# Kernel tuning notes

Hardware: AMD Instinct MI355X
Metric: run time of the kernel (lower is better)

The kernel has to match this reference:

```python
import jax, jax.numpy as jnp
import numpy as np

EPS = 1e-5  # torch BatchNorm1d default eps

def _bn_train(h, gamma, beta):
    # BatchNorm1d in training mode on [B, C] (L=1 after global pool):
    # stats over the batch axis, biased variance.
    mu = h.mean(axis=0)
    var = ((h - mu) ** 2).mean(axis=0)
    return (h - mu) * jax.lax.rsqrt(var + EPS) * gamma + beta

def setup_inputs() -> dict:
    key = jax.random.key(0)
    k_x, k_w1, k_w2 = jax.random.split(key, 3)
    B, C, L = 16, 256, 16384
    Cr = C // 2  # reduction = 2
    x = jax.random.normal(k_x, (B, C, L), dtype=jnp.float32)
    # Conv1d kernel_size=1, bias=False -> channel matmuls; kaiming-ish scale
    w1 = jax.random.normal(k_w1, (Cr, C), dtype=jnp.float32) * (1.0 / np.sqrt(C))
    w2 = jax.random.normal(k_w2, (C, Cr), dtype=jnp.float32) * (1.0 / np.sqrt(Cr))
    g1 = jnp.ones((Cr,), jnp.float32)
    b1 = jnp.zeros((Cr,), jnp.float32)
    g2 = jnp.ones((C,), jnp.float32)
    b2 = jnp.zeros((C,), jnp.float32)
    return {"x": x, "w1": w1, "g1": g1, "b1": b1, "w2": w2, "g2": g2, "b2": b2}

def reference(x, w1, g1, b1, w2, g2, b2):
    # x: [B, C, L]
    s = x.mean(axis=-1)                      # AdaptiveAvgPool1d(1) -> [B, C]
    h = jnp.einsum('bc,rc->br', s, w1)       # 1x1 conv squeeze -> [B, Cr]
    h = _bn_train(h, g1, b1)
    h = jax.nn.gelu(h, approximate=False)    # torch nn.GELU default (erf)
    h = jnp.einsum('br,cr->bc', h, w2)       # 1x1 conv excite -> [B, C]
    h = _bn_train(h, g2, b2)
    gate = jax.nn.sigmoid(h)                 # [B, C]
    return x * gate[:, :, None]              # broadcast multiply over L
```

## Files before the change

kernel.cpp:

```cpp
#include <hip/hip_runtime.h>
#include <math.h>

#define B 16
#define C 256
#define CR 128
#define L 16384
#define NROW (B * C)
#define THREADS 256
#define ITERS (L / 4 / THREADS)

__global__ __launch_bounds__(THREADS) void row_mean_kernel(
    const float* __restrict__ x, float* __restrict__ s) {
    const int row = blockIdx.x;
    const int t = threadIdx.x;
    const float4* xr = (const float4*)(x + (size_t)row * L);

    float acc = 0.0f;
#pragma unroll
    for (int i = 0; i < ITERS; ++i) {
        float4 v = xr[t + i * THREADS];
        acc += (v.x + v.y) + (v.z + v.w);
    }
#pragma unroll
    for (int off = 32; off > 0; off >>= 1) acc += __shfl_down(acc, off, 64);

    __shared__ float wsum[THREADS / 64];
    if ((t & 63) == 0) wsum[t >> 6] = acc;
    __syncthreads();
    if (t == 0) {
        float tot = 0.0f;
#pragma unroll
        for (int w = 0; w < THREADS / 64; ++w) tot += wsum[w];
        s[row] = tot * (1.0f / (float)L);
    }
}

__global__ __launch_bounds__(256) void mlp1_kernel(
    const float* __restrict__ s, const float* __restrict__ w1,
    const float* __restrict__ g1, const float* __restrict__ b1,
    float* __restrict__ h1) {
    const int r = blockIdx.x;
    const int t = threadIdx.x;
    const int b = t >> 4;
    const int j = t & 15;

    const float4* sv = (const float4*)(s + b * C) + j * 4;
    const float4* wv = (const float4*)(w1 + r * C) + j * 4;
    float acc = 0.0f;
#pragma unroll
    for (int k = 0; k < 4; ++k) {
        float4 a = sv[k], w = wv[k];
        acc += a.x * w.x + a.y * w.y + a.z * w.z + a.w * w.w;
    }
#pragma unroll
    for (int off = 8; off > 0; off >>= 1) acc += __shfl_down(acc, off, 16);

    __shared__ float h[B];
    if (j == 0) h[b] = acc;
    __syncthreads();

    float mu = 0.0f;
#pragma unroll
    for (int i = 0; i < B; ++i) mu += h[i];
    mu *= (1.0f / (float)B);
    float var = 0.0f;
#pragma unroll
    for (int i = 0; i < B; ++i) { float d = h[i] - mu; var = fmaf(d, d, var); }
    var *= (1.0f / (float)B);
    const float inv = rsqrtf(var + 1e-5f);

    if (t < B) {
        float v = (h[t] - mu) * inv * g1[r] + b1[r];
        v = 0.5f * v * (1.0f + erff(v * 0.70710678118654752440f));
        h1[t * CR + r] = v;
    }
}

__global__ __launch_bounds__(128) void mlp2_kernel(
    const float* __restrict__ h1, const float* __restrict__ w2,
    const float* __restrict__ g2, const float* __restrict__ b2,
    float* __restrict__ gate) {
    const int c = blockIdx.x;
    const int t = threadIdx.x;
    const int b = t >> 3;
    const int j = t & 7;

    const float4* hv = (const float4*)(h1 + b * CR) + j * 4;
    const float4* wv = (const float4*)(w2 + c * CR) + j * 4;
    float acc = 0.0f;
#pragma unroll
    for (int k = 0; k < 4; ++k) {
        float4 a = hv[k], w = wv[k];
        acc += a.x * w.x + a.y * w.y + a.z * w.z + a.w * w.w;
    }
#pragma unroll
    for (int off = 4; off > 0; off >>= 1) acc += __shfl_down(acc, off, 8);

    __shared__ float h[B];
    if (j == 0) h[b] = acc;
    __syncthreads();

    float mu = 0.0f;
#pragma unroll
    for (int i = 0; i < B; ++i) mu += h[i];
    mu *= (1.0f / (float)B);
    float var = 0.0f;
#pragma unroll
    for (int i = 0; i < B; ++i) { float d = h[i] - mu; var = fmaf(d, d, var); }
    var *= (1.0f / (float)B);
    const float inv = rsqrtf(var + 1e-5f);

    if (t < B) {
        float v = (h[t] - mu) * inv * g2[c] + b2[c];
        gate[t * C + c] = 1.0f / (1.0f + expf(-v));
    }
}

__global__ __launch_bounds__(THREADS) void scale_kernel(
    const float* __restrict__ x, const float* __restrict__ gate,
    float* __restrict__ out) {
    const int row = blockIdx.x;
    const int t = threadIdx.x;
    const float g = gate[row];
    const float4* xr = (const float4*)(x + (size_t)row * L);
    float4* orow = (float4*)(out + (size_t)row * L);
#pragma unroll
    for (int i = 0; i < ITERS; ++i) {
        float4 v = xr[t + i * THREADS];
        v.x *= g; v.y *= g; v.z *= g; v.w *= g;
        orow[t + i * THREADS] = v;
    }
}

extern "C" void kernel_launch(void* const* d_in, const int* in_sizes, int n_in,
                              void* d_out, int out_size, void* d_ws, size_t ws_size,
                              hipStream_t stream) {
    const float* x  = (const float*)d_in[0];
    const float* w1 = (const float*)d_in[1];
    const float* g1 = (const float*)d_in[2];
    const float* b1 = (const float*)d_in[3];
    const float* w2 = (const float*)d_in[4];
    const float* g2 = (const float*)d_in[5];
    const float* b2 = (const float*)d_in[6];
    float* out = (float*)d_out;

    float* s    = (float*)d_ws;
    float* h1   = s + NROW;
    float* gate = h1 + B * CR;

    row_mean_kernel<<<NROW, THREADS, 0, stream>>>(x, s);
    mlp1_kernel<<<CR, 256, 0, stream>>>(s, w1, g1, b1, h1);
    mlp2_kernel<<<C, 128, 0, stream>>>(h1, w2, g2, b2, gate);
    scale_kernel<<<NROW, THREADS, 0, stream>>>(x, gate, out);
}
```

Before: 503.2 us.

## Fuse MLP stages into one block, reverse scale order, nontemporal stores

Merges the two small MLP/BatchNorm kernels into a single one-block kernel that keeps s and h1 in shared memory, which removes a launch and a global round trip. The scale kernel now walks rows in reverse so it first reads the rows the mean pass touched last, which may still be in cache, and it writes its output with nontemporal stores. The risk is that the fused MLP runs on a single workgroup doing serial dot products, which could be slower than the two parallel launches it replaces.

Result: slower. 517.5 us (+2.8%).

```diff
diff --git a/kernel.cpp b/kernel.cpp
--- a/kernel.cpp
+++ b/kernel.cpp
@@ -8,6 +8,8 @@
 #define NROW (B * C)
 #define THREADS 256
 #define ITERS (L / 4 / THREADS)
+
+typedef float v4f __attribute__((ext_vector_type(4)));
 
 __global__ __launch_bounds__(THREADS) void row_mean_kernel(
     const float* __restrict__ x, float* __restrict__ s) {
@@ -35,100 +37,107 @@
     }
 }
 
-__global__ __launch_bounds__(256) void mlp1_kernel(
+__global__ __launch_bounds__(256) void mlp_fused_kernel(
     const float* __restrict__ s, const float* __restrict__ w1,
     const float* __restrict__ g1, const float* __restrict__ b1,
-    float* __restrict__ h1) {
-    const int r = blockIdx.x;
+    const float* __restrict__ w2, const float* __restrict__ g2,
+    const float* __restrict__ b2, float* __restrict__ gate) {
+    __shared__ float s_sh[B][C];
+    __shared__ float h1_sh[B][CR];
     const int t = threadIdx.x;
-    const int b = t >> 4;
-    const int j = t & 15;
 
-    const float4* sv = (const float4*)(s + b * C) + j * 4;
-    const float4* wv = (const float4*)(w1 + r * C) + j * 4;
-    float acc = 0.0f;
-#pragma unroll
-    for (int k = 0; k < 4; ++k) {
-        float4 a = sv[k], w = wv[k];
-        acc += a.x * w.x + a.y * w.y + a.z * w.z + a.w * w.w;
-    }
-#pragma unroll
-    for (int off = 8; off > 0; off >>= 1) acc += __shfl_down(acc, off, 16);
-
-    __shared__ float h[B];
-    if (j == 0) h[b] = acc;
+    for (int i = t; i < B * C; i += 256) s_sh[i >> 8][i & (C - 1)] = s[i];
     __syncthreads();
 
-    float mu = 0.0f;
+    {
+        const int r = t & (CR - 1);
+        const int half = t >> 7;
+        float acc[8];
 #pragma unroll
-    for (int i = 0; i < B; ++i) mu += h[i];
-    mu *= (1.0f / (float)B);
-    float var = 0.0f;
+        for (int bb = 0; bb < 8; ++bb) acc[bb] = 0.0f;
+        for (int k = 0; k < C; k += 4) {
+            float4 w = *(const float4*)(w1 + r * C + k);
 #pragma unroll
-    for (int i = 0; i < B; ++i) { float d = h[i] - mu; var = fmaf(d, d, var); }
-    var *= (1.0f / (float)B);
-    const float inv = rsqrtf(var + 1e-5f);
-
-    if (t < B) {
-        float v = (h[t] - mu) * inv * g1[r] + b1[r];
-        v = 0.5f * v * (1.0f + erff(v * 0.70710678118654752440f));
-        h1[t * CR + r] = v;
+            for (int bb = 0; bb < 8; ++bb) {
+                const float* a = &s_sh[half * 8 + bb][k];
+                acc[bb] = fmaf(a[0], w.x, acc[bb]);
+                acc[bb] = fmaf(a[1], w.y, acc[bb]);
+                acc[bb] = fmaf(a[2], w.z, acc[bb]);
+                acc[bb] = fmaf(a[3], w.w, acc[bb]);
+            }
+        }
+#pragma unroll
+        for (int bb = 0; bb < 8; ++bb) h1_sh[half * 8 + bb][r] = acc[bb];
     }
-}
-
-__global__ __launch_bounds__(128) void mlp2_kernel(
-    const float* __restrict__ h1, const float* __restrict__ w2,
-    const float* __restrict__ g2, const float* __restrict__ b2,
-    float* __restrict__ gate) {
-    const int c = blockIdx.x;
-    const int t = threadIdx.x;
-    const int b = t >> 3;
-    const int j = t & 7;
-
-    const float4* hv = (const float4*)(h1 + b * CR) + j * 4;
-    const float4* wv = (const float4*)(w2 + c * CR) + j * 4;
-    float acc = 0.0f;
-#pragma unroll
-    for (int k = 0; k < 4; ++k) {
-        float4 a = hv[k], w = wv[k];
-        acc += a.x * w.x + a.y * w.y + a.z * w.z + a.w * w.w;
-    }
-#pragma unroll
-    for (int off = 4; off > 0; off >>= 1) acc += __shfl_down(acc, off, 8);
-
-    __shared__ float h[B];
-    if (j == 0) h[b] = acc;
     __syncthreads();
 
-    float mu = 0.0f;
+    if (t < CR) {
+        float mu = 0.0f;
 #pragma unroll
-    for (int i = 0; i < B; ++i) mu += h[i];
-    mu *= (1.0f / (float)B);
-    float var = 0.0f;
+        for (int i = 0; i < B; ++i) mu += h1_sh[i][t];
+        mu *= (1.0f / (float)B);
+        float var = 0.0f;
 #pragma unroll
-    for (int i = 0; i < B; ++i) { float d = h[i] - mu; var = fmaf(d, d, var); }
-    var *= (1.0f / (float)B);
-    const float inv = rsqrtf(var + 1e-5f);
+        for (int i = 0; i < B; ++i) { float d = h1_sh[i][t] - mu; var = fmaf(d, d, var); }
+        var *= (1.0f / (float)B);
+        const float inv = rsqrtf(var + 1e-5f);
+        const float gg = g1[t], bs = b1[t];
+#pragma unroll
+        for (int i = 0; i < B; ++i) {
+            float v = (h1_sh[i][t] - mu) * inv * gg + bs;
+            v = 0.5f * v * (1.0f + erff(v * 0.70710678118654752440f));
+            h1_sh[i][t] = v;
+        }
+    }
+    __syncthreads();
 
-    if (t < B) {
-        float v = (h[t] - mu) * inv * g2[c] + b2[c];
-        gate[t * C + c] = 1.0f / (1.0f + expf(-v));
+    {
+        const int c = t;
+        float acc2[B];
+#pragma unroll
+        for (int i = 0; i < B; ++i) acc2[i] = 0.0f;
+        for (int k = 0; k < CR; k += 4) {
+            float4 w = *(const float4*)(w2 + c * CR + k);
+#pragma unroll
+            for (int i = 0; i < B; ++i) {
+                const float* a = &h1_sh[i][k];
+                acc2[i] = fmaf(a[0], w.x, acc2[i]);
+                acc2[i] = fmaf(a[1], w.y, acc2[i]);
+                acc2[i] = fmaf(a[2], w.z, acc2[i]);
+                acc2[i] = fmaf(a[3], w.w, acc2[i]);
+            }
+        }
+        float mu = 0.0f;
+#pragma unroll
+        for (int i = 0; i < B; ++i) mu += acc2[i];
+        mu *= (1.0f / (float)B);
+        float var = 0.0f;
+#pragma unroll
+        for (int i = 0; i < B; ++i) { float d = acc2[i] - mu; var = fmaf(d, d, var); }
+        var *= (1.0f / (float)B);
+        const float inv = rsqrtf(var + 1e-5f);
+        const float gg = g2[c], bs = b2[c];
+#pragma unroll
+        for (int i = 0; i < B; ++i) {
+            float v = (acc2[i] - mu) * inv * gg + bs;
+            gate[i * C + c] = 1.0f / (1.0f + expf(-v));
+        }
     }
 }
 
 __global__ __launch_bounds__(THREADS) void scale_kernel(
     const float* __restrict__ x, const float* __restrict__ gate,
     float* __restrict__ out) {
-    const int row = blockIdx.x;
+    const int row = NROW - 1 - blockIdx.x;
     const int t = threadIdx.x;
     const float g = gate[row];
-    const float4* xr = (const float4*)(x + (size_t)row * L);
-    float4* orow = (float4*)(out + (size_t)row * L);
+    const v4f* xr = (const v4f*)(x + (size_t)row * L);
+    v4f* orow = (v4f*)(out + (size_t)row * L);
 #pragma unroll
     for (int i = 0; i < ITERS; ++i) {
-        float4 v = xr[t + i * THREADS];
-        v.x *= g; v.y *= g; v.z *= g; v.w *= g;
-        orow[t + i * THREADS] = v;
+        v4f v = xr[t + i * THREADS];
+        v *= g;
+        __builtin_nontemporal_store(v, &orow[t + i * THREADS]);
     }
 }
 
@@ -145,11 +154,9 @@
     float* out = (float*)d_out;
 
     float* s    = (float*)d_ws;
-    float* h1   = s + NROW;
-    float* gate = h1 + B * CR;
+    float* gate = s + NROW;
 
     row_mean_kernel<<<NROW, THREADS, 0, stream>>>(x, s);
-    mlp1_kernel<<<CR, 256, 0, stream>>>(s, w1, g1, b1, h1);
-    mlp2_kernel<<<C, 128, 0, stream>>>(h1, w2, g2, b2, gate);
+    mlp_fused_kernel<<<1, 256, 0, stream>>>(s, w1, g1, b1, w2, g2, b2, gate);
     scale_kernel<<<NROW, THREADS, 0, stream>>>(x, gate, out);
 }
```
